# Kernel optimization log

Measured on AMD Instinct MI355X. Metric: run time of the kernel, lower is better.

Reference implementation:

```python
import jax, jax.numpy as jnp
import numpy as np

G, NPG, DEG = 64, 1024, 16          # graphs, nodes/graph, avg degree
N, E = G * NPG, G * NPG * DEG        # 65536 nodes, 1048576 edges
F, H = 128, 128                      # num_features, n_hidden
K1, K2 = NPG // 2, NPG // 4          # ceil(0.5*1024)=512, ceil(0.5*512)=256


def setup_inputs() -> dict:
    key = jax.random.key(0)
    ks = jax.random.split(key, 16)
    x = jax.random.normal(ks[0], (N, F), dtype=jnp.float32)
    # edges constrained within each graph (block-diagonal adjacency)
    offs = (jnp.arange(G, dtype=jnp.int32) * NPG)[:, None]
    src = (jax.random.randint(ks[1], (G, E // G), 0, NPG, dtype=jnp.int32) + offs).reshape(-1)
    dst = (jax.random.randint(ks[2], (G, E // G), 0, NPG, dtype=jnp.int32) + offs).reshape(-1)
    def lin(k, fi, fo):
        s = 1.0 / np.sqrt(fi)
        return jax.random.uniform(k, (fi, fo), jnp.float32, -s, s)
    return dict(
        x=x, src=src, dst=dst,
        W1=lin(ks[3], F, H),  b1=jnp.zeros((H,), jnp.float32),
        Ws1=lin(ks[4], H, 1), bs1=jnp.zeros((1,), jnp.float32),
        W2=lin(ks[5], H, H),  b2=jnp.zeros((H,), jnp.float32),
        Ws2=lin(ks[6], H, 1), bs2=jnp.zeros((1,), jnp.float32),
        Wl1=lin(ks[7], 2 * H, H), bl1=jnp.zeros((H,), jnp.float32),
        Wl2=lin(ks[8], H, 1),     bl2=jnp.zeros((1,), jnp.float32),
    )


def gcn_conv(x, src, dst, ew, W, b):
    """GCNConv: D^-1/2 (A+I) D^-1/2 (x W) + b, with edge weights ew."""
    n = x.shape[0]
    h = x @ W
    loop = jnp.arange(n, dtype=src.dtype)
    s = jnp.concatenate([src, loop])
    d = jnp.concatenate([dst, loop])
    w = jnp.concatenate([ew, jnp.ones((n,), x.dtype)])
    deg = jax.ops.segment_sum(w, d, num_segments=n)
    dinv = jnp.where(deg > 0, jax.lax.rsqrt(jnp.maximum(deg, 1e-12)), 0.0)
    norm = dinv[s] * dinv[d] * w
    return jax.ops.segment_sum(norm[:, None] * h[s], d, num_segments=n) + b


def sag_pool(x, src, dst, ew, Ws, bs, n_per_graph, k):
    """SAGPooling: GCN attention score, per-graph top-k, x*tanh(score), edge prune via mask."""
    n = x.shape[0]
    g = n // n_per_graph
    score = gcn_conv(x, src, dst, ew, Ws, bs)[:, 0]                 # [n]
    _, idx = jax.lax.top_k(score.reshape(g, n_per_graph), k)        # [g, k]
    perm = (idx + (jnp.arange(g, dtype=jnp.int32) * n_per_graph)[:, None]).reshape(-1)
    xn = x[perm] * jnp.tanh(score[perm])[:, None]                   # [g*k, H]
    kept = jnp.zeros((n,), bool).at[perm].set(True)
    nmap = jnp.zeros((n,), jnp.int32).at[perm].set(jnp.arange(g * k, dtype=jnp.int32))
    valid = kept[src] & kept[dst] & (ew > 0)
    ewn = jnp.where(valid, ew, 0.0)
    srcn = jnp.where(valid, nmap[src], 0)
    dstn = jnp.where(valid, nmap[dst], 0)
    return xn, srcn, dstn, ewn


def reference(x, src, dst, W1, b1, Ws1, bs1, W2, b2, Ws2, bs2, Wl1, bl1, Wl2, bl2):
    ew = jnp.ones((src.shape[0],), x.dtype)
    h = jax.nn.relu(gcn_conv(x, src, dst, ew, W1, b1))
    h, s1, d1, ew1 = sag_pool(h, src, dst, ew, Ws1, bs1, NPG, K1)
    hb = h.reshape(G, K1, H)
    x1 = jnp.concatenate([hb.max(axis=1), hb.mean(axis=1)], axis=1)  # [G, 2H]
    h = jax.nn.relu(gcn_conv(h, s1, d1, ew1, W2, b2))
    h, s2, d2, ew2 = sag_pool(h, s1, d1, ew1, Ws2, bs2, K1, K2)
    hb = h.reshape(G, K2, H)
    x2 = jnp.concatenate([hb.max(axis=1), hb.mean(axis=1)], axis=1)
    z = x1 + x2
    z = jax.nn.relu(z @ Wl1 + bl1)                                  # dropout: eval mode (identity)
    return (z @ Wl2 + bl2)[:, 0]                                     # [G]
```

## Files before the change

kernel.cpp:

```cpp
#include <hip/hip_runtime.h>
#include <math.h>

constexpr int NN1 = 65536;
constexpr int EE  = 1048576;
constexpr int GG  = 64;
constexpr int HH  = 128;
constexpr int NPG = 1024;
constexpr int EPG = 16384;
constexpr int K1  = 512;
constexpr int M1  = GG * K1;
constexpr int K2  = 256;
constexpr int M2  = GG * K2;

__device__ __forceinline__ float4 f4add(float4 a, float4 b)
{
    a.x += b.x; a.y += b.y; a.z += b.z; a.w += b.w; return a;
}

__global__ __launch_bounds__(256) void gemm1_k(const float* __restrict__ A,
                                               const float* __restrict__ W,
                                               const int* __restrict__ rbeg,
                                               const int* __restrict__ rend,
                                               float* __restrict__ C)
{
    __shared__ float Wl[64 * 160];
    const int t    = threadIdx.x;
    const int rowg = t >> 3;
    const int cg   = t & 7;
    const int r0   = (blockIdx.x << 7) + rowg;

    const float* Ar0 = A + ((size_t)r0 << 7);
    const float* Ar1 = Ar0 + (32 << 7);
    const float* Ar2 = Ar1 + (32 << 7);
    const float* Ar3 = Ar2 + (32 << 7);

    float acc[4][16];
#pragma unroll
    for (int i = 0; i < 4; ++i)
#pragma unroll
        for (int j = 0; j < 16; ++j) acc[i][j] = 0.f;

    {
        const float4* Wg = (const float4*)W;
#pragma unroll
        for (int i = 0; i < 8; ++i) {
            int idx = t + (i << 8);
            int k   = idx >> 5;
            int c4  = (idx & 31) << 2;
            *(float4*)&Wl[k * 160 + (c4 >> 4) * 20 + (c4 & 15)] = Wg[idx];
        }
    }
    float4 xc0 = *(const float4*)(Ar0), xc1 = *(const float4*)(Ar1);
    float4 xc2 = *(const float4*)(Ar2), xc3 = *(const float4*)(Ar3);
    __syncthreads();

    const float* wbase = &Wl[cg * 20];

#pragma unroll 1
    for (int k0 = 0; k0 < 64; k0 += 4) {
        float4 xn0 = *(const float4*)(Ar0 + k0 + 4);
        float4 xn1 = *(const float4*)(Ar1 + k0 + 4);
        float4 xn2 = *(const float4*)(Ar2 + k0 + 4);
        float4 xn3 = *(const float4*)(Ar3 + k0 + 4);
#pragma unroll
        for (int kk = 0; kk < 4; ++kk) {
            const float* wr = wbase + (k0 + kk) * 160;
            float x0 = ((const float*)&xc0)[kk], x1 = ((const float*)&xc1)[kk];
            float x2 = ((const float*)&xc2)[kk], x3 = ((const float*)&xc3)[kk];
#pragma unroll
            for (int jh = 0; jh < 16; jh += 8) {
                float wv[8];
                *(float4*)&wv[0] = *(const float4*)(wr + jh);
                *(float4*)&wv[4] = *(const float4*)(wr + jh + 4);
#pragma unroll
                for (int j = 0; j < 8; ++j) {
                    acc[0][jh + j] = fmaf(x0, wv[j], acc[0][jh + j]);
                    acc[1][jh + j] = fmaf(x1, wv[j], acc[1][jh + j]);
                    acc[2][jh + j] = fmaf(x2, wv[j], acc[2][jh + j]);
                    acc[3][jh + j] = fmaf(x3, wv[j], acc[3][jh + j]);
                }
            }
        }
        xc0 = xn0; xc1 = xn1; xc2 = xn2; xc3 = xn3;
    }
    __syncthreads();
    {
        const float4* Wg = (const float4*)(W + 64 * 128);
#pragma unroll
        for (int i = 0; i < 8; ++i) {
            int idx = t + (i << 8);
            int k   = idx >> 5;
            int c4  = (idx & 31) << 2;
            *(float4*)&Wl[k * 160 + (c4 >> 4) * 20 + (c4 & 15)] = Wg[idx];
        }
    }
    __syncthreads();

#pragma unroll 1
    for (int k0 = 64; k0 < 128; k0 += 4) {
        bool pf = (k0 < 124);
        float4 xn0, xn1, xn2, xn3;
        if (pf) {
            xn0 = *(const float4*)(Ar0 + k0 + 4);
            xn1 = *(const float4*)(Ar1 + k0 + 4);
            xn2 = *(const float4*)(Ar2 + k0 + 4);
            xn3 = *(const float4*)(Ar3 + k0 + 4);
        }
#pragma unroll
        for (int kk = 0; kk < 4; ++kk) {
            const float* wr = wbase + (k0 - 64 + kk) * 160;
            float x0 = ((const float*)&xc0)[kk], x1 = ((const float*)&xc1)[kk];
            float x2 = ((const float*)&xc2)[kk], x3 = ((const float*)&xc3)[kk];
#pragma unroll
            for (int jh = 0; jh < 16; jh += 8) {
                float wv[8];
                *(float4*)&wv[0] = *(const float4*)(wr + jh);
                *(float4*)&wv[4] = *(const float4*)(wr + jh + 4);
#pragma unroll
                for (int j = 0; j < 8; ++j) {
                    acc[0][jh + j] = fmaf(x0, wv[j], acc[0][jh + j]);
                    acc[1][jh + j] = fmaf(x1, wv[j], acc[1][jh + j]);
                    acc[2][jh + j] = fmaf(x2, wv[j], acc[2][jh + j]);
                    acc[3][jh + j] = fmaf(x3, wv[j], acc[3][jh + j]);
                }
            }
        }
        if (pf) { xc0 = xn0; xc1 = xn1; xc2 = xn2; xc3 = xn3; }
    }

#pragma unroll
    for (int i = 0; i < 4; ++i) {
        int r = r0 + (i << 5);
        float deg = (float)(rend[r] - rbeg[r]) + 1.0f;
        float sc = 1.0f / sqrtf(deg);
        float* cp = C + ((size_t)r << 7) + (cg << 4);
#pragma unroll
        for (int j = 0; j < 16; j += 4) {
            float4 v;
            v.x = acc[i][j] * sc; v.y = acc[i][j + 1] * sc;
            v.z = acc[i][j + 2] * sc; v.w = acc[i][j + 3] * sc;
            *(float4*)(cp + j) = v;
        }
    }
}

__global__ __launch_bounds__(256) void gemm2_k(const float* __restrict__ A,
                                               const float* __restrict__ W,
                                               const int* __restrict__ rbeg,
                                               const int* __restrict__ rend,
                                               const int* __restrict__ perm,
                                               const float* __restrict__ tsel,
                                               float* __restrict__ C)
{
    __shared__ float Wl[64 * 160];
    const int t    = threadIdx.x;
    const int rowg = t >> 3;
    const int cg   = t & 7;
    const int r0   = (blockIdx.x << 7) + rowg;

    const float* Ar0 = A + ((size_t)perm[r0] << 7);
    const float* Ar1 = A + ((size_t)perm[r0 + 32] << 7);
    const float* Ar2 = A + ((size_t)perm[r0 + 64] << 7);
    const float* Ar3 = A + ((size_t)perm[r0 + 96] << 7);

    float acc[4][16];
#pragma unroll
    for (int i = 0; i < 4; ++i)
#pragma unroll
        for (int j = 0; j < 16; ++j) acc[i][j] = 0.f;

    {
        const float4* Wg = (const float4*)W;
#pragma unroll
        for (int i = 0; i < 8; ++i) {
            int idx = t + (i << 8);
            int k   = idx >> 5;
            int c4  = (idx & 31) << 2;
            *(float4*)&Wl[k * 160 + (c4 >> 4) * 20 + (c4 & 15)] = Wg[idx];
        }
    }
    float4 xc0 = *(const float4*)(Ar0), xc1 = *(const float4*)(Ar1);
    float4 xc2 = *(const float4*)(Ar2), xc3 = *(const float4*)(Ar3);
    __syncthreads();

    const float* wbase = &Wl[cg * 20];

#pragma unroll 1
    for (int k0 = 0; k0 < 64; k0 += 4) {
        float4 xn0 = *(const float4*)(Ar0 + k0 + 4);
        float4 xn1 = *(const float4*)(Ar1 + k0 + 4);
        float4 xn2 = *(const float4*)(Ar2 + k0 + 4);
        float4 xn3 = *(const float4*)(Ar3 + k0 + 4);
#pragma unroll
        for (int kk = 0; kk < 4; ++kk) {
            const float* wr = wbase + (k0 + kk) * 160;
            float x0 = ((const float*)&xc0)[kk], x1 = ((const float*)&xc1)[kk];
            float x2 = ((const float*)&xc2)[kk], x3 = ((const float*)&xc3)[kk];
#pragma unroll
            for (int jh = 0; jh < 16; jh += 8) {
                float wv[8];
                *(float4*)&wv[0] = *(const float4*)(wr + jh);
                *(float4*)&wv[4] = *(const float4*)(wr + jh + 4);
#pragma unroll
                for (int j = 0; j < 8; ++j) {
                    acc[0][jh + j] = fmaf(x0, wv[j], acc[0][jh + j]);
                    acc[1][jh + j] = fmaf(x1, wv[j], acc[1][jh + j]);
                    acc[2][jh + j] = fmaf(x2, wv[j], acc[2][jh + j]);
                    acc[3][jh + j] = fmaf(x3, wv[j], acc[3][jh + j]);
                }
            }
        }
        xc0 = xn0; xc1 = xn1; xc2 = xn2; xc3 = xn3;
    }
    __syncthreads();
    {
        const float4* Wg = (const float4*)(W + 64 * 128);
#pragma unroll
        for (int i = 0; i < 8; ++i) {
            int idx = t + (i << 8);
            int k   = idx >> 5;
            int c4  = (idx & 31) << 2;
            *(float4*)&Wl[k * 160 + (c4 >> 4) * 20 + (c4 & 15)] = Wg[idx];
        }
    }
    __syncthreads();

#pragma unroll 1
    for (int k0 = 64; k0 < 128; k0 += 4) {
        bool pf = (k0 < 124);
        float4 xn0, xn1, xn2, xn3;
        if (pf) {
            xn0 = *(const float4*)(Ar0 + k0 + 4);
            xn1 = *(const float4*)(Ar1 + k0 + 4);
            xn2 = *(const float4*)(Ar2 + k0 + 4);
            xn3 = *(const float4*)(Ar3 + k0 + 4);
        }
#pragma unroll
        for (int kk = 0; kk < 4; ++kk) {
            const float* wr = wbase + (k0 - 64 + kk) * 160;
            float x0 = ((const float*)&xc0)[kk], x1 = ((const float*)&xc1)[kk];
            float x2 = ((const float*)&xc2)[kk], x3 = ((const float*)&xc3)[kk];
#pragma unroll
            for (int jh = 0; jh < 16; jh += 8) {
                float wv[8];
                *(float4*)&wv[0] = *(const float4*)(wr + jh);
                *(float4*)&wv[4] = *(const float4*)(wr + jh + 4);
#pragma unroll
                for (int j = 0; j < 8; ++j) {
                    acc[0][jh + j] = fmaf(x0, wv[j], acc[0][jh + j]);
                    acc[1][jh + j] = fmaf(x1, wv[j], acc[1][jh + j]);
                    acc[2][jh + j] = fmaf(x2, wv[j], acc[2][jh + j]);
                    acc[3][jh + j] = fmaf(x3, wv[j], acc[3][jh + j]);
                }
            }
        }
        if (pf) { xc0 = xn0; xc1 = xn1; xc2 = xn2; xc3 = xn3; }
    }

#pragma unroll
    for (int i = 0; i < 4; ++i) {
        int r = r0 + (i << 5);
        float deg = (float)(rend[r] - rbeg[r]) + 1.0f;
        float sc = tsel[r] / sqrtf(deg);
        float* cp = C + ((size_t)r << 7) + (cg << 4);
#pragma unroll
        for (int j = 0; j < 16; j += 4) {
            float4 v;
            v.x = acc[i][j] * sc; v.y = acc[i][j + 1] * sc;
            v.z = acc[i][j + 2] * sc; v.w = acc[i][j + 3] * sc;
            *(float4*)(cp + j) = v;
        }
    }
}

__global__ __launch_bounds__(1024) void build_csr1_k(const int* __restrict__ src, const int* __restrict__ dst,
                                                     int* __restrict__ rbeg, int* __restrict__ rend,
                                                     int* __restrict__ csr)
{
    __shared__ int cnt[NPG];
    int t = threadIdx.x, g = blockIdx.x;
    int ebase = g * EPG;
    cnt[t] = 0;
    __syncthreads();
#pragma unroll
    for (int k = 0; k < EPG / 1024; ++k) {
        int d = dst[ebase + t + k * 1024] & (NPG - 1);
        atomicAdd(&cnt[d], 1);
    }
    __syncthreads();
    int deg0 = cnt[t];
    int val = deg0;
    for (int off = 1; off < NPG; off <<= 1) {
        int u = (t >= off) ? cnt[t - off] : 0;
        __syncthreads();
        val += u; cnt[t] = val;
        __syncthreads();
    }
    int node = g * NPG + t;
    rbeg[node] = ebase + val - deg0;
    rend[node] = ebase + val;
    cnt[t] = val - deg0;
    __syncthreads();
#pragma unroll
    for (int k = 0; k < EPG / 1024; ++k) {
        int e = ebase + t + k * 1024;
        int d = dst[e] & (NPG - 1);
        int pos = atomicAdd(&cnt[d], 1);
        csr[ebase + pos] = src[e];
    }
}

__global__ __launch_bounds__(1024) void build_csr2_k(const int* __restrict__ src, const int* __restrict__ dst,
                                                     const int* __restrict__ nmap,
                                                     int* __restrict__ rbeg, int* __restrict__ rend,
                                                     int* __restrict__ csr)
{
    __shared__ int cnt[K1];
    int t = threadIdx.x, g = blockIdx.x;
    int ebase = g * EPG;
    if (t < K1) cnt[t] = 0;
    __syncthreads();
    int ns[EPG / 1024], nd[EPG / 1024];
#pragma unroll
    for (int k = 0; k < EPG / 1024; ++k) {
        int e = ebase + t + k * 1024;
        ns[k] = nmap[src[e]];
        nd[k] = nmap[dst[e]];
        if (ns[k] >= 0 && nd[k] >= 0) atomicAdd(&cnt[nd[k] & (K1 - 1)], 1);
    }
    __syncthreads();
    int deg0 = 0, val = 0;
    if (t < K1) { deg0 = cnt[t]; val = deg0; }
    for (int off = 1; off < K1; off <<= 1) {
        int u = (t < K1 && t >= off) ? cnt[t - off] : 0;
        __syncthreads();
        if (t < K1) { val += u; cnt[t] = val; }
        __syncthreads();
    }
    if (t < K1) {
        int node = g * K1 + t;
        rbeg[node] = ebase + val - deg0;
        rend[node] = ebase + val;
        cnt[t] = val - deg0;
    }
    __syncthreads();
#pragma unroll
    for (int k = 0; k < EPG / 1024; ++k) {
        if (ns[k] >= 0 && nd[k] >= 0) {
            int pos = atomicAdd(&cnt[nd[k] & (K1 - 1)], 1);
            csr[ebase + pos] = ns[k];
        }
    }
}

__global__ __launch_bounds__(256) void agg_feat_k(const float4* __restrict__ XWs,
                                                  const int* __restrict__ rbeg, const int* __restrict__ rend,
                                                  const int* __restrict__ csr,
                                                  const float* __restrict__ bias, const float* __restrict__ Ws,
                                                  float* __restrict__ hout, float* __restrict__ hss, int n)
{
    int nblk = gridDim.x;
    int bid  = blockIdx.x;
    int b    = (bid & 7) * (nblk >> 3) + (bid >> 3);
    int half = threadIdx.x >> 5;
    int lane = threadIdx.x & 31;
    int node = (b << 3) + half;
    if (node >= n) return;
    const float4* Xf = XWs + lane;

    float4 A = make_float4(0.f, 0.f, 0.f, 0.f), B = A, C = A, D = A;
    int p0 = rbeg[node], p1 = rend[node];
    int p = p0;
    for (; p + 8 <= p1; p += 8) {
        int s0 = csr[p], s1 = csr[p + 1], s2 = csr[p + 2], s3 = csr[p + 3];
        int s4 = csr[p + 4], s5 = csr[p + 5], s6 = csr[p + 6], s7 = csr[p + 7];
        float4 v0 = Xf[(size_t)s0 << 5], v1 = Xf[(size_t)s1 << 5];
        float4 v2 = Xf[(size_t)s2 << 5], v3 = Xf[(size_t)s3 << 5];
        float4 v4 = Xf[(size_t)s4 << 5], v5 = Xf[(size_t)s5 << 5];
        float4 v6 = Xf[(size_t)s6 << 5], v7 = Xf[(size_t)s7 << 5];
        A = f4add(A, v0); B = f4add(B, v1); C = f4add(C, v2); D = f4add(D, v3);
        A = f4add(A, v4); B = f4add(B, v5); C = f4add(C, v6); D = f4add(D, v7);
    }
    for (; p + 4 <= p1; p += 4) {
        int s0 = csr[p], s1 = csr[p + 1], s2 = csr[p + 2], s3 = csr[p + 3];
        float4 v0 = Xf[(size_t)s0 << 5], v1 = Xf[(size_t)s1 << 5];
        float4 v2 = Xf[(size_t)s2 << 5], v3 = Xf[(size_t)s3 << 5];
        A = f4add(A, v0); B = f4add(B, v1); C = f4add(C, v2); D = f4add(D, v3);
    }
    for (; p < p1; ++p) {
        int s = csr[p];
        A = f4add(A, Xf[(size_t)s << 5]);
    }
    float4 acc = f4add(f4add(A, B), f4add(C, D));
    acc = f4add(acc, Xf[(size_t)node << 5]);

    float dd = 1.0f / sqrtf((float)(p1 - p0) + 1.0f);
    float4 bb = *(const float4*)(bias + (lane << 2));
    acc.x = fmaxf(fmaf(acc.x, dd, bb.x), 0.f);
    acc.y = fmaxf(fmaf(acc.y, dd, bb.y), 0.f);
    acc.z = fmaxf(fmaf(acc.z, dd, bb.z), 0.f);
    acc.w = fmaxf(fmaf(acc.w, dd, bb.w), 0.f);
    *(float4*)(hout + ((size_t)node << 7) + (lane << 2)) = acc;

    float4 wsv = *(const float4*)(Ws + (lane << 2));
    float pq = acc.x * wsv.x + acc.y * wsv.y + acc.z * wsv.z + acc.w * wsv.w;
#pragma unroll
    for (int off = 16; off > 0; off >>= 1) pq += __shfl_down(pq, off, 32);
    if (lane == 0) hss[node] = dd * pq;
}

template <int NNE, int KK, bool MARK>
__global__ void sctopk_k(const int* __restrict__ rbeg, const int* __restrict__ rend,
                         const int* __restrict__ csr, const float* __restrict__ hss,
                         const float* __restrict__ bsp,
                         int* __restrict__ perm, float* __restrict__ tsel,
                         int* __restrict__ nmap)
{
    __shared__ unsigned long long keys[NNE];
    int t = threadIdx.x, g = blockIdx.x;
    int node = g * NNE + t;
    int p0 = rbeg[node], p1 = rend[node];
    float a = 0.f, b = 0.f, c = 0.f, e = 0.f;
    int p = p0;
    for (; p + 8 <= p1; p += 8) {
        int s0 = csr[p], s1 = csr[p + 1], s2 = csr[p + 2], s3 = csr[p + 3];
        int s4 = csr[p + 4], s5 = csr[p + 5], s6 = csr[p + 6], s7 = csr[p + 7];
        a += hss[s0]; b += hss[s1]; c += hss[s2]; e += hss[s3];
        a += hss[s4]; b += hss[s5]; c += hss[s6]; e += hss[s7];
    }
    for (; p + 4 <= p1; p += 4) {
        int s0 = csr[p], s1 = csr[p + 1], s2 = csr[p + 2], s3 = csr[p + 3];
        a += hss[s0]; b += hss[s1]; c += hss[s2]; e += hss[s3];
    }
    for (; p < p1; ++p) a += hss[csr[p]];
    float dd = 1.0f / sqrtf((float)(p1 - p0) + 1.0f);
    float s = fmaf((a + b) + (c + e) + hss[node], dd, bsp[0]);

    unsigned u = __float_as_uint(s);
    u = (u & 0x80000000u) ? ~u : (u | 0x80000000u);
    keys[t] = (((unsigned long long)u) << 32) | (unsigned)(NNE - 1 - t);
    __syncthreads();
    for (int k = 2; k <= NNE; k <<= 1) {
        for (int j = k >> 1; j > 0; j >>= 1) {
            int ixj = t ^ j;
            if (ixj > t) {
                unsigned long long ka = keys[t], kb = keys[ixj];
                bool up = ((t & k) == 0);
                if ((ka > kb) == up) { keys[t] = kb; keys[ixj] = ka; }
            }
            __syncthreads();
        }
    }
    unsigned long long key = keys[NNE - 1 - t];
    int idx = NNE - 1 - (int)(key & 0xFFFFFFFFu);
    if (t < KK) {
        perm[g * KK + t] = g * NNE + idx;
        unsigned uu = (unsigned)(key >> 32);
        float sc = __uint_as_float((uu & 0x80000000u) ? (uu ^ 0x80000000u) : ~uu);
        tsel[g * KK + t] = tanhf(sc);
        if (MARK) nmap[g * NNE + idx] = g * KK + t;
    } else if (MARK) {
        nmap[g * NNE + idx] = -1;
    }
}

__global__ __launch_bounds__(128) void readout_ix_k(const float* __restrict__ h,
                                                    const int* __restrict__ perm,
                                                    const float* __restrict__ tsel,
                                                    float* __restrict__ part)
{
    int b = blockIdx.x, t = threadIdx.x;
    int base = b * 128;
    float mx = -INFINITY, sm = 0.f;
#pragma unroll 4
    for (int r = 0; r < 128; ++r) {
        int o = perm[base + r];
        float tv = tsel[base + r];
        float v = h[((size_t)o << 7) + t] * tv;
        mx = fmaxf(mx, v);
        sm += v;
    }
    part[b * 256 + t] = mx;
    part[b * 256 + 128 + t] = sm;
}

__global__ __launch_bounds__(128) void mlp_k(const float* __restrict__ part1, const float* __restrict__ part2,
                                             const float* __restrict__ Wl1, const float* __restrict__ bl1,
                                             const float* __restrict__ Wl2, const float* __restrict__ bl2,
                                             float* __restrict__ out)
{
    __shared__ float z[256];
    __shared__ float red[128];
    int g = blockIdx.x, t = threadIdx.x;
    float mx1 = -INFINITY, sm1 = 0.f;
#pragma unroll
    for (int j = 0; j < 4; ++j) {
        mx1 = fmaxf(mx1, part1[(g * 4 + j) * 256 + t]);
        sm1 += part1[(g * 4 + j) * 256 + 128 + t];
    }
    float mx2 = -INFINITY, sm2 = 0.f;
#pragma unroll
    for (int j = 0; j < 2; ++j) {
        mx2 = fmaxf(mx2, part2[(g * 2 + j) * 256 + t]);
        sm2 += part2[(g * 2 + j) * 256 + 128 + t];
    }
    z[t]       = mx1 + mx2;
    z[t + 128] = sm1 * (1.f / 512.f) + sm2 * (1.f / 256.f);
    __syncthreads();
    float acc = bl1[t];
    for (int k = 0; k < 256; ++k) acc = fmaf(z[k], Wl1[k * 128 + t], acc);
    float zz = fmaxf(acc, 0.f);
    red[t] = zz * Wl2[t];
    __syncthreads();
    for (int off = 64; off > 0; off >>= 1) {
        if (t < off) red[t] += red[t + off];
        __syncthreads();
    }
    if (t == 0) out[g] = red[0] + bl2[0];
}

extern "C" void kernel_launch(void* const* d_in, const int* in_sizes, int n_in,
                              void* d_out, int out_size, void* d_ws, size_t ws_size,
                              hipStream_t stream)
{
    const float* x   = (const float*)d_in[0];
    const int*   src = (const int*)d_in[1];
    const int*   dst = (const int*)d_in[2];
    const float* W1  = (const float*)d_in[3];
    const float* b1  = (const float*)d_in[4];
    const float* Ws1 = (const float*)d_in[5];
    const float* bs1 = (const float*)d_in[6];
    const float* W2  = (const float*)d_in[7];
    const float* b2  = (const float*)d_in[8];
    const float* Ws2 = (const float*)d_in[9];
    const float* bs2 = (const float*)d_in[10];
    const float* Wl1 = (const float*)d_in[11];
    const float* bl1 = (const float*)d_in[12];
    const float* Wl2 = (const float*)d_in[13];
    const float* bl2 = (const float*)d_in[14];
    float* out = (float*)d_out;
    char* ws = (char*)d_ws;

    float* XW1 = (float*)(ws);
    float* h1  = (float*)(ws + ((size_t)32 << 20));
    float* XW2 = (float*)(ws);
    float* h2  = (float*)(ws + ((size_t)16 << 20));
    size_t SB = (size_t)64 << 20;
    auto alloc = [&](size_t bytes) { char* p = ws + SB; SB += (bytes + 255) & ~(size_t)255; return p; };
    int* csr1     = (int*)alloc((size_t)EE * 4);
    int* rbeg1    = (int*)alloc(NN1 * 4);
    int* rend1    = (int*)alloc(NN1 * 4);
    float* hss1   = (float*)alloc(NN1 * 4);
    int* nmap     = (int*)alloc(NN1 * 4);
    int* perm1    = (int*)alloc(M1 * 4);
    float* tsel1  = (float*)alloc(M1 * 4);
    int* rbeg2    = (int*)alloc(M1 * 4);
    int* rend2    = (int*)alloc(M1 * 4);
    float* hss2   = (float*)alloc(M1 * 4);
    int* perm2    = (int*)alloc(M2 * 4);
    float* tsel2  = (float*)alloc(M2 * 4);
    float* part1  = (float*)alloc(256 * 256 * 4);
    float* part2  = (float*)alloc(128 * 256 * 4);
    int* csr2     = csr1;
    (void)ws_size; (void)in_sizes; (void)n_in; (void)out_size;

    build_csr1_k<<<GG, 1024, 0, stream>>>(src, dst, rbeg1, rend1, csr1);
    gemm1_k<<<NN1 / 128, 256, 0, stream>>>(x, W1, rbeg1, rend1, XW1);
    agg_feat_k<<<NN1 / 8, 256, 0, stream>>>((const float4*)XW1, rbeg1, rend1, csr1, b1, Ws1, h1, hss1, NN1);
    sctopk_k<NPG, K1, true><<<GG, NPG, 0, stream>>>(rbeg1, rend1, csr1, hss1, bs1, perm1, tsel1, nmap);
    build_csr2_k<<<GG, 1024, 0, stream>>>(src, dst, nmap, rbeg2, rend2, csr2);
    gemm2_k<<<M1 / 128, 256, 0, stream>>>(h1, W2, rbeg2, rend2, perm1, tsel1, XW2);
    readout_ix_k<<<M1 / 128, 128, 0, stream>>>(h1, perm1, tsel1, part1);
    agg_feat_k<<<M1 / 8, 256, 0, stream>>>((const float4*)XW2, rbeg2, rend2, csr2, b2, Ws2, h2, hss2, M1);
    sctopk_k<K1, K2, false><<<GG, K1, 0, stream>>>(rbeg2, rend2, csr2, hss2, bs2, perm2, tsel2, nullptr);
    readout_ix_k<<<M2 / 128, 128, 0, stream>>>(h2, perm2, tsel2, part2);
    mlp_k<<<GG, 128, 0, stream>>>(part1, part2, Wl1, bl1, Wl2, bl2, out);
}
```

Baseline: 216.2 us.

## Fuse pooled CSR rebuild into score/top-k kernel and stage scores in LDS

The separate build_csr2 kernel is folded into the tail of the first score/top-k kernel. The node remap now lives in shared memory, so the global nmap buffer and one kernel launch go away. Neighbour score gathers in the top-k kernel now read a per-graph shared-memory copy of hss, using locally masked indices, instead of global memory. This adds several extra barriers and more work per block in the fused kernel, and it relies on every edge staying inside its own graph.

Measured after the change: 208.3 us. -3.7%, faster.

```diff
diff --git a/kernel.cpp b/kernel.cpp
--- a/kernel.cpp
+++ b/kernel.cpp
@@ -307,49 +307,6 @@
         int d = dst[e] & (NPG - 1);
         int pos = atomicAdd(&cnt[d], 1);
         csr[ebase + pos] = src[e];
-    }
-}
-
-__global__ __launch_bounds__(1024) void build_csr2_k(const int* __restrict__ src, const int* __restrict__ dst,
-                                                     const int* __restrict__ nmap,
-                                                     int* __restrict__ rbeg, int* __restrict__ rend,
-                                                     int* __restrict__ csr)
-{
-    __shared__ int cnt[K1];
-    int t = threadIdx.x, g = blockIdx.x;
-    int ebase = g * EPG;
-    if (t < K1) cnt[t] = 0;
-    __syncthreads();
-    int ns[EPG / 1024], nd[EPG / 1024];
-#pragma unroll
-    for (int k = 0; k < EPG / 1024; ++k) {
-        int e = ebase + t + k * 1024;
-        ns[k] = nmap[src[e]];
-        nd[k] = nmap[dst[e]];
-        if (ns[k] >= 0 && nd[k] >= 0) atomicAdd(&cnt[nd[k] & (K1 - 1)], 1);
-    }
-    __syncthreads();
-    int deg0 = 0, val = 0;
-    if (t < K1) { deg0 = cnt[t]; val = deg0; }
-    for (int off = 1; off < K1; off <<= 1) {
-        int u = (t < K1 && t >= off) ? cnt[t - off] : 0;
-        __syncthreads();
-        if (t < K1) { val += u; cnt[t] = val; }
-        __syncthreads();
-    }
-    if (t < K1) {
-        int node = g * K1 + t;
-        rbeg[node] = ebase + val - deg0;
-        rend[node] = ebase + val;
-        cnt[t] = val - deg0;
-    }
-    __syncthreads();
-#pragma unroll
-    for (int k = 0; k < EPG / 1024; ++k) {
-        if (ns[k] >= 0 && nd[k] >= 0) {
-            int pos = atomicAdd(&cnt[nd[k] & (K1 - 1)], 1);
-            csr[ebase + pos] = ns[k];
-        }
     }
 }
 
@@ -409,35 +366,45 @@
     if (lane == 0) hss[node] = dd * pq;
 }
 
-template <int NNE, int KK, bool MARK>
+template <int NNE, int KK, bool BUILD>
 __global__ void sctopk_k(const int* __restrict__ rbeg, const int* __restrict__ rend,
                          const int* __restrict__ csr, const float* __restrict__ hss,
                          const float* __restrict__ bsp,
                          int* __restrict__ perm, float* __restrict__ tsel,
-                         int* __restrict__ nmap)
+                         const int* __restrict__ src, const int* __restrict__ dst,
+                         int* __restrict__ rbeg2, int* __restrict__ rend2,
+                         int* __restrict__ csr2)
 {
     __shared__ unsigned long long keys[NNE];
+    __shared__ float hl[NNE];
     int t = threadIdx.x, g = blockIdx.x;
     int node = g * NNE + t;
+    hl[t] = hss[node];
+    __syncthreads();
+
     int p0 = rbeg[node], p1 = rend[node];
     float a = 0.f, b = 0.f, c = 0.f, e = 0.f;
     int p = p0;
     for (; p + 8 <= p1; p += 8) {
-        int s0 = csr[p], s1 = csr[p + 1], s2 = csr[p + 2], s3 = csr[p + 3];
-        int s4 = csr[p + 4], s5 = csr[p + 5], s6 = csr[p + 6], s7 = csr[p + 7];
-        a += hss[s0]; b += hss[s1]; c += hss[s2]; e += hss[s3];
-        a += hss[s4]; b += hss[s5]; c += hss[s6]; e += hss[s7];
+        int s0 = csr[p] & (NNE - 1), s1 = csr[p + 1] & (NNE - 1);
+        int s2 = csr[p + 2] & (NNE - 1), s3 = csr[p + 3] & (NNE - 1);
+        int s4 = csr[p + 4] & (NNE - 1), s5 = csr[p + 5] & (NNE - 1);
+        int s6 = csr[p + 6] & (NNE - 1), s7 = csr[p + 7] & (NNE - 1);
+        a += hl[s0]; b += hl[s1]; c += hl[s2]; e += hl[s3];
+        a += hl[s4]; b += hl[s5]; c += hl[s6]; e += hl[s7];
     }
     for (; p + 4 <= p1; p += 4) {
-        int s0 = csr[p], s1 = csr[p + 1], s2 = csr[p + 2], s3 = csr[p + 3];
-        a += hss[s0]; b += hss[s1]; c += hss[s2]; e += hss[s3];
-    }
-    for (; p < p1; ++p) a += hss[csr[p]];
+        int s0 = csr[p] & (NNE - 1), s1 = csr[p + 1] & (NNE - 1);
+        int s2 = csr[p + 2] & (NNE - 1), s3 = csr[p + 3] & (NNE - 1);
+        a += hl[s0]; b += hl[s1]; c += hl[s2]; e += hl[s3];
+    }
+    for (; p < p1; ++p) a += hl[csr[p] & (NNE - 1)];
     float dd = 1.0f / sqrtf((float)(p1 - p0) + 1.0f);
-    float s = fmaf((a + b) + (c + e) + hss[node], dd, bsp[0]);
+    float s = fmaf((a + b) + (c + e) + hl[t], dd, bsp[0]);
 
     unsigned u = __float_as_uint(s);
     u = (u & 0x80000000u) ? ~u : (u | 0x80000000u);
+    __syncthreads();
     keys[t] = (((unsigned long long)u) << 32) | (unsigned)(NNE - 1 - t);
     __syncthreads();
     for (int k = 2; k <= NNE; k <<= 1) {
@@ -458,9 +425,51 @@
         unsigned uu = (unsigned)(key >> 32);
         float sc = __uint_as_float((uu & 0x80000000u) ? (uu ^ 0x80000000u) : ~uu);
         tsel[g * KK + t] = tanhf(sc);
-        if (MARK) nmap[g * NNE + idx] = g * KK + t;
-    } else if (MARK) {
-        nmap[g * NNE + idx] = -1;
+    }
+
+    if (BUILD) {
+        constexpr int EPT = BUILD ? (EPG / NNE) : 1;
+        __syncthreads();
+        int* nml = (int*)hl;
+        int* cnt = (int*)keys;
+        nml[t] = -1;
+        if (t < KK) cnt[t] = 0;
+        __syncthreads();
+        if (t < KK) nml[idx] = t;
+        __syncthreads();
+
+        int ebase = g * EPG;
+        int nsl[EPT], ndl[EPT];
+#pragma unroll
+        for (int k = 0; k < EPT; ++k) {
+            int e = ebase + t + k * NNE;
+            nsl[k] = nml[src[e] & (NNE - 1)];
+            ndl[k] = nml[dst[e] & (NNE - 1)];
+            if (nsl[k] >= 0 && ndl[k] >= 0) atomicAdd(&cnt[ndl[k]], 1);
+        }
+        __syncthreads();
+        int deg0 = 0, val = 0;
+        if (t < KK) { deg0 = cnt[t]; val = deg0; }
+        for (int off = 1; off < KK; off <<= 1) {
+            int u2 = (t < KK && t >= off) ? cnt[t - off] : 0;
+            __syncthreads();
+            if (t < KK) { val += u2; cnt[t] = val; }
+            __syncthreads();
+        }
+        if (t < KK) {
+            int n2 = g * KK + t;
+            rbeg2[n2] = ebase + val - deg0;
+            rend2[n2] = ebase + val;
+            cnt[t] = val - deg0;
+        }
+        __syncthreads();
+#pragma unroll
+        for (int k = 0; k < EPT; ++k) {
+            if (nsl[k] >= 0 && ndl[k] >= 0) {
+                int pos = atomicAdd(&cnt[ndl[k]], 1);
+                csr2[ebase + pos] = g * KK + nsl[k];
+            }
+        }
     }
 }
 
@@ -551,7 +560,6 @@
     int* rbeg1    = (int*)alloc(NN1 * 4);
     int* rend1    = (int*)alloc(NN1 * 4);
     float* hss1   = (float*)alloc(NN1 * 4);
-    int* nmap     = (int*)alloc(NN1 * 4);
     int* perm1    = (int*)alloc(M1 * 4);
     float* tsel1  = (float*)alloc(M1 * 4);
     int* rbeg2    = (int*)alloc(M1 * 4);
@@ -567,12 +575,13 @@
     build_csr1_k<<<GG, 1024, 0, stream>>>(src, dst, rbeg1, rend1, csr1);
     gemm1_k<<<NN1 / 128, 256, 0, stream>>>(x, W1, rbeg1, rend1, XW1);
     agg_feat_k<<<NN1 / 8, 256, 0, stream>>>((const float4*)XW1, rbeg1, rend1, csr1, b1, Ws1, h1, hss1, NN1);
-    sctopk_k<NPG, K1, true><<<GG, NPG, 0, stream>>>(rbeg1, rend1, csr1, hss1, bs1, perm1, tsel1, nmap);
-    build_csr2_k<<<GG, 1024, 0, stream>>>(src, dst, nmap, rbeg2, rend2, csr2);
+    sctopk_k<NPG, K1, true><<<GG, NPG, 0, stream>>>(rbeg1, rend1, csr1, hss1, bs1, perm1, tsel1,
+                                                    src, dst, rbeg2, rend2, csr2);
     gemm2_k<<<M1 / 128, 256, 0, stream>>>(h1, W2, rbeg2, rend2, perm1, tsel1, XW2);
     readout_ix_k<<<M1 / 128, 128, 0, stream>>>(h1, perm1, tsel1, part1);
     agg_feat_k<<<M1 / 8, 256, 0, stream>>>((const float4*)XW2, rbeg2, rend2, csr2, b2, Ws2, h2, hss2, M1);
-    sctopk_k<K1, K2, false><<<GG, K1, 0, stream>>>(rbeg2, rend2, csr2, hss2, bs2, perm2, tsel2, nullptr);
+    sctopk_k<K1, K2, false><<<GG, K1, 0, stream>>>(rbeg2, rend2, csr2, hss2, bs2, perm2, tsel2,
+                                                   nullptr, nullptr, nullptr, nullptr, nullptr);
     readout_ix_k<<<M2 / 128, 128, 0, stream>>>(h2, perm2, tsel2, part2);
     mlp_k<<<GG, 128, 0, stream>>>(part1, part2, Wl1, bl1, Wl2, bl2, out);
 }
```
